# Performance work log

Hardware: AMD Instinct MI355X
Metric: run time of the kernel (lower is better)

Reference implementation:

```python
import jax, jax.numpy as jnp
import numpy as np

B, S, D_MODEL, D_K, D_V = 4, 2048, 1024, 1024, 1024


def setup_inputs() -> dict:
    key = jax.random.key(0)
    k1, k2, k3, k4 = jax.random.split(key, 4)
    scale = 1.0 / np.sqrt(D_MODEL)
    x = jax.random.normal(k1, (B, S, D_MODEL), dtype=jnp.float32)
    Wq = jax.random.normal(k2, (D_K, D_MODEL), dtype=jnp.float32) * scale
    Wk = jax.random.normal(k3, (D_K, D_MODEL), dtype=jnp.float32) * scale
    Wv = jax.random.normal(k4, (D_V, D_MODEL), dtype=jnp.float32) * scale
    # causal mask: position i may attend to j <= i (True = keep)
    mask = jnp.broadcast_to(jnp.tril(jnp.ones((S, S), dtype=bool)), (B, S, S))
    return {"x": x, "mask": mask, "Wq": Wq, "Wk": Wk, "Wv": Wv}


def reference(x, mask, Wq, Wk, Wv):
    # nn.Linear(d, k, bias=False): y = x @ W.T with W of shape [k, d]
    q = jnp.einsum('bsd,kd->bsk', x, Wq)
    k = jnp.einsum('bsd,kd->bsk', x, Wk)
    v = jnp.einsum('bsd,vd->bsv', x, Wv)
    scores = jnp.einsum('bik,bjk->bij', q, k) / jnp.sqrt(jnp.float32(D_K))
    s = jnp.where(mask, scores, -jnp.inf)
    # masked, fully-masked-row-safe softmax (fully masked rows -> all zeros,
    # matching softmax[all-masked rows] = 0 in the original)
    m = jnp.max(s, axis=-1, keepdims=True)
    m_safe = jnp.where(jnp.isfinite(m), m, 0.0)
    e = jnp.exp(s - m_safe)          # exp(-inf) = 0 for masked entries
    denom = jnp.sum(e, axis=-1, keepdims=True)
    p = e / jnp.where(denom == 0.0, 1.0, denom)
    return jnp.einsum('bij,bjv->biv', p, v)
```

## Files before the change

### kernel.cpp

```cpp
#include <hip/hip_runtime.h>
#include <hip/hip_bf16.h>
#include <stdint.h>

#define SEQ   2048
#define DM    1024
#define NBAT  4

typedef __attribute__((ext_vector_type(8))) short  short8;
typedef __attribute__((ext_vector_type(4))) float  floatx4;

__device__ __forceinline__ unsigned short f2b(float f) {
    __hip_bfloat16 h = __float2bfloat16(f);
    unsigned short r;
    __builtin_memcpy(&r, &h, 2);
    return r;
}

__device__ __forceinline__ ushort4 pack4(float a, float b, float c, float d) {
    ushort4 u; u.x = f2b(a); u.y = f2b(b); u.z = f2b(c); u.w = f2b(d); return u;
}

__device__ __forceinline__ void gload16(const void* g, void* s) {
    __builtin_amdgcn_global_load_lds(
        (const __attribute__((address_space(1))) unsigned int*)(uintptr_t)g,
        (__attribute__((address_space(3))) unsigned int*)(uintptr_t)s,
        16, 0, 0);
}

__global__ void prep(const float4* __restrict__ x,
                     const float4* __restrict__ w0, const float4* __restrict__ w1,
                     const float4* __restrict__ w2,
                     ushort4* __restrict__ xb, ushort4* __restrict__ wall,
                     float* __restrict__ rsum)
{
    const int b = blockIdx.x;
    const int t = threadIdx.x;
    if (b < 8192) {
        const int i = b * 256 + t;
        float4 f = x[i];
        xb[i] = pack4(f.x, f.y, f.z, f.w);
    } else if (b < 11264) {
        const int idx  = b - 8192;
        const int wsel = idx >> 10;
        const int i    = (idx & 1023) * 256 + t;
        const float4* src = (wsel == 0) ? w0 : (wsel == 1) ? w1 : w2;
        float4 f = src[i];
        wall[(size_t)wsel * 262144 + i] = pack4(f.x, f.y, f.z, f.w);
    } else {
        rsum[(b - 11264) * 256 + t] = 0.f;
    }
}

__global__ __launch_bounds__(256) void qkv_gemm(
    const unsigned short* __restrict__ A, const unsigned short* __restrict__ Bm,
    unsigned short* __restrict__ Qo, unsigned short* __restrict__ Ko,
    unsigned short* __restrict__ Vto, float qscale)
{
    const int m0 = blockIdx.y * 128;
    const int n0 = blockIdx.x * 128;
    const int K  = DM;

    __shared__ __align__(16) unsigned short As[128 * 64];
    __shared__ __align__(16) unsigned short Bs[128 * 64];

    const int t    = threadIdx.x;
    const int w    = t >> 6;
    const int lane = t & 63;
    const int wr   = w >> 1, wc = w & 1;
    const int r    = lane & 15, q = lane >> 4;

    floatx4 acc[4][4];
#pragma unroll
    for (int i = 0; i < 4; i++)
#pragma unroll
        for (int j = 0; j < 4; j++)
            acc[i][j] = (floatx4){0.f, 0.f, 0.f, 0.f};

    const int rr0 = t >> 3;
    const int pg  = (t & 7) ^ ((t >> 3) & 7);
    const int swz = r & 7;

    for (int k0 = 0; k0 < K; k0 += 64) {
        const size_t ka = (size_t)k0 + pg * 8;
#pragma unroll
        for (int g = 0; g < 4; g++) {
            gload16(A  + (size_t)(m0 + g * 32 + rr0) * K + ka, As + g * 2048 + (size_t)w * 512);
            gload16(Bm + (size_t)(n0 + g * 32 + rr0) * K + ka, Bs + g * 2048 + (size_t)w * 512);
        }
        __builtin_amdgcn_s_waitcnt(0);
        __syncthreads();

#pragma unroll
        for (int kk = 0; kk < 2; kk++) {
            short8 af[4], bf[4];
            const int slot = ((kk * 4 + q) ^ swz) * 8;
#pragma unroll
            for (int i = 0; i < 4; i++) {
                af[i] = *(const short8*)&As[(wr * 64 + i * 16 + r) * 64 + slot];
                bf[i] = *(const short8*)&Bs[(wc * 64 + i * 16 + r) * 64 + slot];
            }
#pragma unroll
            for (int i = 0; i < 4; i++)
#pragma unroll
                for (int j = 0; j < 4; j++)
                    acc[i][j] = __builtin_amdgcn_mfma_f32_16x16x32_bf16(af[i], bf[j], acc[i][j], 0, 0, 0);
        }
        __syncthreads();
    }

    const int gmb = m0 + wr * 64 + q * 4;
    const int gnb = n0 + wc * 64 + r;
#pragma unroll
    for (int i = 0; i < 4; i++) {
        const int gm = gmb + i * 16;
#pragma unroll
        for (int j = 0; j < 4; j++) {
            const int gn = gnb + j * 16;
            if (n0 < 1024) {
#pragma unroll
                for (int rr = 0; rr < 4; rr++)
                    Qo[(size_t)(gm + rr) * 1024 + gn] = f2b(acc[i][j][rr] * qscale);
            } else if (n0 < 2048) {
#pragma unroll
                for (int rr = 0; rr < 4; rr++)
                    Ko[(size_t)(gm + rr) * 1024 + (gn - 1024)] = f2b(acc[i][j][rr]);
            } else {
                const int b = gm >> 11;
                const int s = gm & 2047;
                const int v = gn - 2048;
                *(ushort4*)&Vto[((size_t)(b * 1024 + v)) * 2048 + s] =
                    pack4(acc[i][j][0], acc[i][j][1], acc[i][j][2], acc[i][j][3]);
            }
        }
    }
}

template<int MODE>
__global__ __launch_bounds__(256) void attn64(
    const unsigned short* __restrict__ Ag, const unsigned short* __restrict__ Bg,
    void* __restrict__ Cv, float* __restrict__ rowsum)
{
    const int z = blockIdx.z;
    int m0, n0;
    if (MODE == 0) {
        const int f = blockIdx.x;
        int ti = (int)((sqrtf(4.f * f + 1.f) - 1.f) * 0.5f);
        while ((ti + 1) * (ti + 2) <= f) ti++;
        while (ti * (ti + 1) > f) ti--;
        const int tj = f - ti * (ti + 1);
        m0 = ti * 128;
        n0 = tj * 64;
    } else {
        m0 = (int)(gridDim.y - 1 - blockIdx.y) * 128;
        n0 = blockIdx.x * 64;
    }

    const int lda = (MODE == 0) ? DM : SEQ;
    const int ldb = (MODE == 0) ? DM : SEQ;
    const unsigned short* A  = Ag + (size_t)z * ((MODE == 0) ? SEQ * DM : SEQ * SEQ);
    const unsigned short* Bm = Bg + (size_t)z * ((MODE == 0) ? SEQ * DM : DM * SEQ);
    const int kEnd = (MODE == 0) ? DM : (m0 + 128);

    __shared__ __align__(16) unsigned short As[128 * 64];
    __shared__ __align__(16) unsigned short Bs[64 * 64];

    const int t    = threadIdx.x;
    const int w    = t >> 6;
    const int lane = t & 63;
    const int r    = lane & 15, q = lane >> 4;

    floatx4 acc[2][4];
#pragma unroll
    for (int i = 0; i < 2; i++)
#pragma unroll
        for (int j = 0; j < 4; j++)
            acc[i][j] = (floatx4){0.f, 0.f, 0.f, 0.f};

    const int rr0 = t >> 3;
    const int pg  = (t & 7) ^ ((t >> 3) & 7);
    const int swz = r & 7;

    for (int k0 = 0; k0 < kEnd; k0 += 64) {
        const size_t ka = (size_t)k0 + pg * 8;
#pragma unroll
        for (int g = 0; g < 4; g++)
            gload16(A + (size_t)(m0 + g * 32 + rr0) * lda + ka,
                    As + g * 2048 + (size_t)w * 512);
#pragma unroll
        for (int g = 0; g < 2; g++)
            gload16(Bm + (size_t)(n0 + g * 32 + rr0) * ldb + ka,
                    Bs + g * 2048 + (size_t)w * 512);
        __builtin_amdgcn_s_waitcnt(0);
        __syncthreads();

#pragma unroll
        for (int kk = 0; kk < 2; kk++) {
            short8 af[2], bf[4];
            const int slot = ((kk * 4 + q) ^ swz) * 8;
#pragma unroll
            for (int i = 0; i < 2; i++)
                af[i] = *(const short8*)&As[(w * 32 + i * 16 + r) * 64 + slot];
#pragma unroll
            for (int j = 0; j < 4; j++)
                bf[j] = *(const short8*)&Bs[(j * 16 + r) * 64 + slot];
#pragma unroll
            for (int i = 0; i < 2; i++)
#pragma unroll
                for (int j = 0; j < 4; j++)
                    acc[i][j] = __builtin_amdgcn_mfma_f32_16x16x32_bf16(bf[j], af[i], acc[i][j], 0, 0, 0);
        }
        __syncthreads();
    }

    const int gmb = m0 + w * 32 + r;
    const int gnb = n0 + q * 4;
    if (MODE == 0) {
        unsigned short* E = (unsigned short*)Cv + (size_t)z * SEQ * SEQ;
        float* rs = rowsum + (size_t)z * SEQ;
#pragma unroll
        for (int i = 0; i < 2; i++) {
            const int gm = gmb + i * 16;
            float part = 0.f;
#pragma unroll
            for (int j = 0; j < 4; j++) {
                const int gn = gnb + j * 16;
                float e0 = (gn + 0 <= gm) ? __expf(acc[i][j][0]) : 0.f;
                float e1 = (gn + 1 <= gm) ? __expf(acc[i][j][1]) : 0.f;
                float e2 = (gn + 2 <= gm) ? __expf(acc[i][j][2]) : 0.f;
                float e3 = (gn + 3 <= gm) ? __expf(acc[i][j][3]) : 0.f;
                part += (e0 + e1) + (e2 + e3);
                *(ushort4*)&E[(size_t)gm * SEQ + gn] = pack4(e0, e1, e2, e3);
            }
            part += __shfl_xor(part, 16, 64);
            part += __shfl_xor(part, 32, 64);
            if (q == 0) atomicAdd(&rs[gm], part);
        }
    } else {
        float* C = (float*)Cv + (size_t)z * SEQ * DM;
        const float* rs = rowsum + (size_t)z * SEQ;
#pragma unroll
        for (int i = 0; i < 2; i++) {
            const int gm = gmb + i * 16;
            const float inv = 1.0f / rs[gm];
#pragma unroll
            for (int j = 0; j < 4; j++) {
                const int gn = gnb + j * 16;
                float4 o;
                o.x = acc[i][j][0] * inv;
                o.y = acc[i][j][1] * inv;
                o.z = acc[i][j][2] * inv;
                o.w = acc[i][j][3] * inv;
                *(float4*)&C[(size_t)gm * DM + gn] = o;
            }
        }
    }
}

extern "C" void kernel_launch(void* const* d_in, const int* in_sizes, int n_in,
                              void* d_out, int out_size, void* d_ws, size_t ws_size,
                              hipStream_t stream) {
    (void)in_sizes; (void)n_in; (void)out_size; (void)ws_size;
    const float* x  = (const float*)d_in[0];
    const float* Wq = (const float*)d_in[2];
    const float* Wk = (const float*)d_in[3];
    const float* Wv = (const float*)d_in[4];

    char* base = (char*)d_ws;
    size_t off = 0;
    auto alloc = [&](size_t n) { char* p = base + off; off += (n + 255) & ~(size_t)255; return p; };

    unsigned short* xb   = (unsigned short*)alloc((size_t)NBAT * SEQ * DM * 2);
    unsigned short* wall = (unsigned short*)alloc((size_t)3 * DM * DM * 2);
    unsigned short* Qb   = (unsigned short*)alloc((size_t)NBAT * SEQ * DM * 2);
    unsigned short* Kb   = (unsigned short*)alloc((size_t)NBAT * SEQ * DM * 2);
    unsigned short* Vtb  = (unsigned short*)alloc((size_t)NBAT * DM * SEQ * 2);
    unsigned short* E    = (unsigned short*)alloc((size_t)NBAT * SEQ * SEQ * 2);
    float*          rsum = (float*)alloc((size_t)NBAT * SEQ * 4);

    const dim3 blk(256);

    prep<<<dim3(11296), blk, 0, stream>>>(
        (const float4*)x, (const float4*)Wq, (const float4*)Wk, (const float4*)Wv,
        (ushort4*)xb, (ushort4*)wall, rsum);

    const int Mtot = NBAT * SEQ;

    qkv_gemm<<<dim3(3 * DM / 128, Mtot / 128, 1), blk, 0, stream>>>(
        xb, wall, Qb, Kb, Vtb, 0.03125f);

    attn64<0><<<dim3(272, 1, NBAT), blk, 0, stream>>>(Qb, Kb, E, rsum);

    attn64<1><<<dim3(DM / 64, SEQ / 128, NBAT), blk, 0, stream>>>(E, Vtb, d_out, rsum);
}
```

Before: 284.3 us.

## Rewrite QKV GEMM as 256x256 tile, 8-wave, double-buffered pipelined kernel

Replaces the 128x128 single-buffered QKV projection GEMM with a 256x256 tile run by 512 threads. The kernel double-buffers its LDS stages, interleaves async global->LDS loads with the MFMA phases, and uses s_setprio with split barriers. It also adds an XCD-aware block remapping and a new swizzle. The goal is to hide global load latency, raise reuse per loaded byte, and stop stalling on waitcnt(0) every k step. In exchange it uses 128KB of LDS and more registers per thread, and depends on the hand-tuned vmcnt counts being correct.

```diff
diff --git a/kernel.cpp b/kernel.cpp
--- a/kernel.cpp
+++ b/kernel.cpp
@@ -51,83 +51,150 @@
     }
 }
 
-__global__ __launch_bounds__(256) void qkv_gemm(
+__global__ __launch_bounds__(512, 2) void qkv_gemm(
     const unsigned short* __restrict__ A, const unsigned short* __restrict__ Bm,
     unsigned short* __restrict__ Qo, unsigned short* __restrict__ Ko,
     unsigned short* __restrict__ Vto, float qscale)
 {
-    const int m0 = blockIdx.y * 128;
-    const int n0 = blockIdx.x * 128;
-    const int K  = DM;
-
-    __shared__ __align__(16) unsigned short As[128 * 64];
-    __shared__ __align__(16) unsigned short Bs[128 * 64];
+    __shared__ __align__(16) unsigned short lds[65536];
+
+    const int bid = blockIdx.x;
+    const int wg  = (bid & 7) * 48 + (bid >> 3);
+    const int mt  = wg / 12, nt = wg - mt * 12;
+    const int m0  = mt * 256, n0 = nt * 256;
 
     const int t    = threadIdx.x;
     const int w    = t >> 6;
     const int lane = t & 63;
-    const int wr   = w >> 1, wc = w & 1;
+    const int wr   = w >> 2, wc = w & 3;
     const int r    = lane & 15, q = lane >> 4;
 
-    floatx4 acc[4][4];
-#pragma unroll
-    for (int i = 0; i < 4; i++)
+    const int frA = r * 32 + ((q ^ (r & 3) ^ ((r >> 2) & 3)) << 3);
+
+    const int srow = w * 32 + (lane >> 2);
+    const int spc  = ((lane & 3) ^ ((lane >> 2) & 3) ^ (lane >> 4)) << 3;
+
+    floatx4 acc[8][4];
+#pragma unroll
+    for (int i = 0; i < 8; i++)
 #pragma unroll
         for (int j = 0; j < 4; j++)
             acc[i][j] = (floatx4){0.f, 0.f, 0.f, 0.f};
 
-    const int rr0 = t >> 3;
-    const int pg  = (t & 7) ^ ((t >> 3) & 7);
-    const int swz = r & 7;
-
-    for (int k0 = 0; k0 < K; k0 += 64) {
-        const size_t ka = (size_t)k0 + pg * 8;
-#pragma unroll
-        for (int g = 0; g < 4; g++) {
-            gload16(A  + (size_t)(m0 + g * 32 + rr0) * K + ka, As + g * 2048 + (size_t)w * 512);
-            gload16(Bm + (size_t)(n0 + g * 32 + rr0) * K + ka, Bs + g * 2048 + (size_t)w * 512);
-        }
-        __builtin_amdgcn_s_waitcnt(0);
-        __syncthreads();
-
-#pragma unroll
-        for (int kk = 0; kk < 2; kk++) {
-            short8 af[4], bf[4];
-            const int slot = ((kk * 4 + q) ^ swz) * 8;
-#pragma unroll
-            for (int i = 0; i < 4; i++) {
-                af[i] = *(const short8*)&As[(wr * 64 + i * 16 + r) * 64 + slot];
-                bf[i] = *(const short8*)&Bs[(wc * 64 + i * 16 + r) * 64 + slot];
-            }
-#pragma unroll
-            for (int i = 0; i < 4; i++)
-#pragma unroll
-                for (int j = 0; j < 4; j++)
-                    acc[i][j] = __builtin_amdgcn_mfma_f32_16x16x32_bf16(af[i], bf[j], acc[i][j], 0, 0, 0);
-        }
-        __syncthreads();
-    }
-
-    const int gmb = m0 + wr * 64 + q * 4;
+    short8 bf0, bf1, bf2, bf3;
+
+#define APL(P,KH) (((P)*2+(KH)) * 8192)
+#define BPL(P,KH) (32768 + ((P)*2+(KH)) * 8192)
+
+#define STG(G, R0, KB, PL) do { \
+    gload16((G) + (((size_t)((R0) + srow))      << 10) + (KB) + spc, &lds[(PL) + (w*2+0)*512]); \
+    gload16((G) + (((size_t)((R0) + srow + 16)) << 10) + (KB) + spc, &lds[(PL) + (w*2+1)*512]); \
+  } while (0)
+
+#define PHASE(P, KH, MS, SG, SR0, SKB, SPL, DO_VM) do { \
+    const unsigned short* Ap = &lds[APL(P,KH)]; \
+    short8 af0 = *(const short8*)&Ap[((wr)*128 + (MS)*64 +  0)*32 + frA]; \
+    short8 af1 = *(const short8*)&Ap[((wr)*128 + (MS)*64 + 16)*32 + frA]; \
+    short8 af2 = *(const short8*)&Ap[((wr)*128 + (MS)*64 + 32)*32 + frA]; \
+    short8 af3 = *(const short8*)&Ap[((wr)*128 + (MS)*64 + 48)*32 + frA]; \
+    if ((MS) == 0) { \
+        const unsigned short* Bp = &lds[BPL(P,KH)]; \
+        bf0 = *(const short8*)&Bp[((wc)*64 +  0)*32 + frA]; \
+        bf1 = *(const short8*)&Bp[((wc)*64 + 16)*32 + frA]; \
+        bf2 = *(const short8*)&Bp[((wc)*64 + 32)*32 + frA]; \
+        bf3 = *(const short8*)&Bp[((wc)*64 + 48)*32 + frA]; \
+    } \
+    STG(SG, SR0, SKB, SPL); \
+    __builtin_amdgcn_s_barrier(); \
+    asm volatile("s_waitcnt lgkmcnt(0)" ::: "memory"); \
+    __builtin_amdgcn_s_setprio(1); \
+    acc[(MS)*4+0][0] = __builtin_amdgcn_mfma_f32_16x16x32_bf16(af0, bf0, acc[(MS)*4+0][0], 0, 0, 0); \
+    acc[(MS)*4+0][1] = __builtin_amdgcn_mfma_f32_16x16x32_bf16(af0, bf1, acc[(MS)*4+0][1], 0, 0, 0); \
+    acc[(MS)*4+0][2] = __builtin_amdgcn_mfma_f32_16x16x32_bf16(af0, bf2, acc[(MS)*4+0][2], 0, 0, 0); \
+    acc[(MS)*4+0][3] = __builtin_amdgcn_mfma_f32_16x16x32_bf16(af0, bf3, acc[(MS)*4+0][3], 0, 0, 0); \
+    acc[(MS)*4+1][0] = __builtin_amdgcn_mfma_f32_16x16x32_bf16(af1, bf0, acc[(MS)*4+1][0], 0, 0, 0); \
+    acc[(MS)*4+1][1] = __builtin_amdgcn_mfma_f32_16x16x32_bf16(af1, bf1, acc[(MS)*4+1][1], 0, 0, 0); \
+    acc[(MS)*4+1][2] = __builtin_amdgcn_mfma_f32_16x16x32_bf16(af1, bf2, acc[(MS)*4+1][2], 0, 0, 0); \
+    acc[(MS)*4+1][3] = __builtin_amdgcn_mfma_f32_16x16x32_bf16(af1, bf3, acc[(MS)*4+1][3], 0, 0, 0); \
+    acc[(MS)*4+2][0] = __builtin_amdgcn_mfma_f32_16x16x32_bf16(af2, bf0, acc[(MS)*4+2][0], 0, 0, 0); \
+    acc[(MS)*4+2][1] = __builtin_amdgcn_mfma_f32_16x16x32_bf16(af2, bf1, acc[(MS)*4+2][1], 0, 0, 0); \
+    acc[(MS)*4+2][2] = __builtin_amdgcn_mfma_f32_16x16x32_bf16(af2, bf2, acc[(MS)*4+2][2], 0, 0, 0); \
+    acc[(MS)*4+2][3] = __builtin_amdgcn_mfma_f32_16x16x32_bf16(af2, bf3, acc[(MS)*4+2][3], 0, 0, 0); \
+    acc[(MS)*4+3][0] = __builtin_amdgcn_mfma_f32_16x16x32_bf16(af3, bf0, acc[(MS)*4+3][0], 0, 0, 0); \
+    acc[(MS)*4+3][1] = __builtin_amdgcn_mfma_f32_16x16x32_bf16(af3, bf1, acc[(MS)*4+3][1], 0, 0, 0); \
+    acc[(MS)*4+3][2] = __builtin_amdgcn_mfma_f32_16x16x32_bf16(af3, bf2, acc[(MS)*4+3][2], 0, 0, 0); \
+    acc[(MS)*4+3][3] = __builtin_amdgcn_mfma_f32_16x16x32_bf16(af3, bf3, acc[(MS)*4+3][3], 0, 0, 0); \
+    __builtin_amdgcn_s_setprio(0); \
+    if (DO_VM) asm volatile("s_waitcnt vmcnt(8)" ::: "memory"); \
+    __builtin_amdgcn_s_barrier(); \
+  } while (0)
+
+#define TILE(P, KB1, KB2) do { \
+    PHASE(P, 0, 0, A,  m0, (KB1) + 32, APL(1-(P),1), 0); \
+    PHASE(P, 0, 1, Bm, n0, (KB1) + 32, BPL(1-(P),1), 1); \
+    PHASE(P, 1, 0, A,  m0, (KB2),      APL(P,0),     0); \
+    PHASE(P, 1, 1, Bm, n0, (KB2),      BPL(P,0),     1); \
+  } while (0)
+
+    STG(A,  m0, 0,  APL(0,0));
+    STG(Bm, n0, 0,  BPL(0,0));
+    STG(A,  m0, 32, APL(0,1));
+    STG(Bm, n0, 32, BPL(0,1));
+    STG(A,  m0, 64, APL(1,0));
+    STG(Bm, n0, 64, BPL(1,0));
+    asm volatile("s_waitcnt vmcnt(8)" ::: "memory");
+    __builtin_amdgcn_s_barrier();
+
+    for (int tt = 0; tt < 16; tt += 2) {
+        const int kb1a = (tt + 1) * 64;
+        const int kb2a = (tt + 2 < 16 ? tt + 2 : 0) * 64;
+        TILE(0, kb1a, kb2a);
+        const int kb1b = kb2a;
+        const int kb2b = (tt + 3 < 16 ? tt + 3 : tt - 13) * 64;
+        TILE(1, kb1b, kb2b);
+    }
+
+#undef TILE
+#undef PHASE
+#undef STG
+#undef APL
+#undef BPL
+
+    const int gmb = m0 + wr * 128 + q * 4;
     const int gnb = n0 + wc * 64 + r;
-#pragma unroll
-    for (int i = 0; i < 4; i++) {
-        const int gm = gmb + i * 16;
-#pragma unroll
-        for (int j = 0; j < 4; j++) {
-            const int gn = gnb + j * 16;
-            if (n0 < 1024) {
+    if (nt < 4) {
+#pragma unroll
+        for (int i = 0; i < 8; i++) {
+            const int gm = gmb + i * 16;
+#pragma unroll
+            for (int j = 0; j < 4; j++) {
+                const int gn = gnb + j * 16;
 #pragma unroll
                 for (int rr = 0; rr < 4; rr++)
                     Qo[(size_t)(gm + rr) * 1024 + gn] = f2b(acc[i][j][rr] * qscale);
-            } else if (n0 < 2048) {
+            }
+        }
+    } else if (nt < 8) {
+#pragma unroll
+        for (int i = 0; i < 8; i++) {
+            const int gm = gmb + i * 16;
+#pragma unroll
+            for (int j = 0; j < 4; j++) {
+                const int gn = gnb + j * 16;
 #pragma unroll
                 for (int rr = 0; rr < 4; rr++)
                     Ko[(size_t)(gm + rr) * 1024 + (gn - 1024)] = f2b(acc[i][j][rr]);
-            } else {
-                const int b = gm >> 11;
-                const int s = gm & 2047;
-                const int v = gn - 2048;
+            }
+        }
+    } else {
+#pragma unroll
+        for (int i = 0; i < 8; i++) {
+            const int gm = gmb + i * 16;
+            const int b  = gm >> 11;
+            const int s  = gm & 2047;
+#pragma unroll
+            for (int j = 0; j < 4; j++) {
+                const int v = gnb + j * 16 - 2048;
                 *(ushort4*)&Vto[((size_t)(b * 1024 + v)) * 2048 + s] =
                     pack4(acc[i][j][0], acc[i][j][1], acc[i][j][2], acc[i][j][3]);
             }
@@ -283,9 +350,7 @@
         (const float4*)x, (const float4*)Wq, (const float4*)Wk, (const float4*)Wv,
         (ushort4*)xb, (ushort4*)wall, rsum);
 
-    const int Mtot = NBAT * SEQ;
-
-    qkv_gemm<<<dim3(3 * DM / 128, Mtot / 128, 1), blk, 0, stream>>>(
+    qkv_gemm<<<dim3(384), dim3(512), 0, stream>>>(
         xb, wall, Qb, Kb, Vtb, 0.03125f);
 
     attn64<0><<<dim3(272, 1, NBAT), blk, 0, stream>>>(Qb, Kb, E, rsum);
```

After: 283.7 us. About the same (-0.2%).

## Restructure QKV GEMM with 256x128 tiles, 512 threads and 5-stage LDS pipeline

Applied to the files above, without the earlier changes.

The QKV projection GEMM now uses 512-thread blocks computing 256x128 output tiles. A 5-slot LDS ring buffer prefetches four K-steps of 32 ahead with global_load_lds, and waits use explicit vmcnt counts instead of a full drain. Blocks are remapped with an XCD-aware swizzle over a 1D grid, the LDS layout uses a new XOR swizzle, and s_setprio is raised around the MFMA burst. The aim is to hide global-load latency and improve L2 reuse, at the cost of much more LDS per block (about 120KB) and possibly lower occupancy.

```diff
diff --git a/kernel.cpp b/kernel.cpp
--- a/kernel.cpp
+++ b/kernel.cpp
@@ -51,17 +51,19 @@
     }
 }
 
-__global__ __launch_bounds__(256) void qkv_gemm(
+#define SLOT 12288
+
+__global__ __launch_bounds__(512, 2) void qkv_gemm(
     const unsigned short* __restrict__ A, const unsigned short* __restrict__ Bm,
     unsigned short* __restrict__ Qo, unsigned short* __restrict__ Ko,
     unsigned short* __restrict__ Vto, float qscale)
 {
-    const int m0 = blockIdx.y * 128;
-    const int n0 = blockIdx.x * 128;
-    const int K  = DM;
-
-    __shared__ __align__(16) unsigned short As[128 * 64];
-    __shared__ __align__(16) unsigned short Bs[128 * 64];
+    __shared__ __align__(16) unsigned short lds[5 * SLOT];
+
+    const int bid = blockIdx.x;
+    const int wg  = (bid & 7) * 96 + (bid >> 3);
+    const int mt  = wg / 24, nt = wg - mt * 24;
+    const int m0  = mt * 256, n0 = nt * 128;
 
     const int t    = threadIdx.x;
     const int w    = t >> 6;
@@ -69,6 +71,16 @@
     const int wr   = w >> 1, wc = w & 1;
     const int r    = lane & 15, q = lane >> 4;
 
+    const int rp      = (r & ~1) | ((r ^ (r >> 1)) & 1);
+    const int fr      = (r & 3) ^ ((r >> 2) & 3);
+    const int laneOff = rp * 32 + ((q ^ fr) << 3);
+
+    const int R   = t >> 2;
+    const int sR  = (R & ~1) | ((R ^ (R >> 1)) & 1);
+    const int fS  = (sR & 3) ^ ((sR >> 2) & 3);
+    const int jS  = ((t & 3) ^ fS) << 3;
+    const int wS  = w * 512;
+
     floatx4 acc[4][4];
 #pragma unroll
     for (int i = 0; i < 4; i++)
@@ -76,58 +88,102 @@
         for (int j = 0; j < 4; j++)
             acc[i][j] = (floatx4){0.f, 0.f, 0.f, 0.f};
 
-    const int rr0 = t >> 3;
-    const int pg  = (t & 7) ^ ((t >> 3) & 7);
-    const int swz = r & 7;
-
-    for (int k0 = 0; k0 < K; k0 += 64) {
-        const size_t ka = (size_t)k0 + pg * 8;
-#pragma unroll
-        for (int g = 0; g < 4; g++) {
-            gload16(A  + (size_t)(m0 + g * 32 + rr0) * K + ka, As + g * 2048 + (size_t)w * 512);
-            gload16(Bm + (size_t)(n0 + g * 32 + rr0) * K + ka, Bs + g * 2048 + (size_t)w * 512);
-        }
-        __builtin_amdgcn_s_waitcnt(0);
-        __syncthreads();
-
-#pragma unroll
-        for (int kk = 0; kk < 2; kk++) {
-            short8 af[4], bf[4];
-            const int slot = ((kk * 4 + q) ^ swz) * 8;
-#pragma unroll
-            for (int i = 0; i < 4; i++) {
-                af[i] = *(const short8*)&As[(wr * 64 + i * 16 + r) * 64 + slot];
-                bf[i] = *(const short8*)&Bs[(wc * 64 + i * 16 + r) * 64 + slot];
-            }
-#pragma unroll
-            for (int i = 0; i < 4; i++)
-#pragma unroll
-                for (int j = 0; j < 4; j++)
-                    acc[i][j] = __builtin_amdgcn_mfma_f32_16x16x32_bf16(af[i], bf[j], acc[i][j], 0, 0, 0);
-        }
-        __syncthreads();
-    }
+#define STG3(T4, DSTS) do { \
+    const int kb_ = ((T4) < 32) ? (T4) * 32 : 0; \
+    gload16(A  + (((size_t)(m0 +       sR)) << 10) + kb_ + jS, &lds[(DSTS) +        wS]); \
+    gload16(A  + (((size_t)(m0 + 128 + sR)) << 10) + kb_ + jS, &lds[(DSTS) + 4096 + wS]); \
+    gload16(Bm + (((size_t)(n0 +       sR)) << 10) + kb_ + jS, &lds[(DSTS) + 8192 + wS]); \
+  } while (0)
+
+    STG3(0, 0 * SLOT);
+    STG3(1, 1 * SLOT);
+    STG3(2, 2 * SLOT);
+    STG3(3, 3 * SLOT);
+    asm volatile("s_waitcnt vmcnt(9)" ::: "memory");
+    __builtin_amdgcn_s_barrier();
+
+    int p = 0, q4 = 4;
+    for (int tt = 0; tt < 32; ++tt) {
+        const int slotS = p * SLOT;
+        const int aBase = slotS + wr * 4096 + laneOff;
+        const int aB = slotS + (wr >> 1) * 4096 + (wr & 1) * 2048 + laneOff;
+        const int bB = slotS + 8192 + wc * 2048 + laneOff;
+        (void)aBase;
+
+        short8 af0 = *(const short8*)&lds[aB +    0];
+        short8 af1 = *(const short8*)&lds[aB +  512];
+        short8 af2 = *(const short8*)&lds[aB + 1024];
+        short8 af3 = *(const short8*)&lds[aB + 1536];
+        short8 bf0 = *(const short8*)&lds[bB +    0];
+        short8 bf1 = *(const short8*)&lds[bB +  512];
+        short8 bf2 = *(const short8*)&lds[bB + 1024];
+        short8 bf3 = *(const short8*)&lds[bB + 1536];
+
+        STG3(tt + 4, q4 * SLOT);
+
+        asm volatile("s_waitcnt vmcnt(9)" ::: "memory");
+        __builtin_amdgcn_s_barrier();
+        asm volatile("s_waitcnt lgkmcnt(0)" ::: "memory");
+        __builtin_amdgcn_s_setprio(1);
+        acc[0][0] = __builtin_amdgcn_mfma_f32_16x16x32_bf16(af0, bf0, acc[0][0], 0, 0, 0);
+        acc[0][1] = __builtin_amdgcn_mfma_f32_16x16x32_bf16(af0, bf1, acc[0][1], 0, 0, 0);
+        acc[0][2] = __builtin_amdgcn_mfma_f32_16x16x32_bf16(af0, bf2, acc[0][2], 0, 0, 0);
+        acc[0][3] = __builtin_amdgcn_mfma_f32_16x16x32_bf16(af0, bf3, acc[0][3], 0, 0, 0);
+        acc[1][0] = __builtin_amdgcn_mfma_f32_16x16x32_bf16(af1, bf0, acc[1][0], 0, 0, 0);
+        acc[1][1] = __builtin_amdgcn_mfma_f32_16x16x32_bf16(af1, bf1, acc[1][1], 0, 0, 0);
+        acc[1][2] = __builtin_amdgcn_mfma_f32_16x16x32_bf16(af1, bf2, acc[1][2], 0, 0, 0);
+        acc[1][3] = __builtin_amdgcn_mfma_f32_16x16x32_bf16(af1, bf3, acc[1][3], 0, 0, 0);
+        acc[2][0] = __builtin_amdgcn_mfma_f32_16x16x32_bf16(af2, bf0, acc[2][0], 0, 0, 0);
+        acc[2][1] = __builtin_amdgcn_mfma_f32_16x16x32_bf16(af2, bf1, acc[2][1], 0, 0, 0);
+        acc[2][2] = __builtin_amdgcn_mfma_f32_16x16x32_bf16(af2, bf2, acc[2][2], 0, 0, 0);
+        acc[2][3] = __builtin_amdgcn_mfma_f32_16x16x32_bf16(af2, bf3, acc[2][3], 0, 0, 0);
+        acc[3][0] = __builtin_amdgcn_mfma_f32_16x16x32_bf16(af3, bf0, acc[3][0], 0, 0, 0);
+        acc[3][1] = __builtin_amdgcn_mfma_f32_16x16x32_bf16(af3, bf1, acc[3][1], 0, 0, 0);
+        acc[3][2] = __builtin_amdgcn_mfma_f32_16x16x32_bf16(af3, bf2, acc[3][2], 0, 0, 0);
+        acc[3][3] = __builtin_amdgcn_mfma_f32_16x16x32_bf16(af3, bf3, acc[3][3], 0, 0, 0);
+        __builtin_amdgcn_s_setprio(0);
+        __builtin_amdgcn_s_barrier();
+
+        p  = (p  == 4) ? 0 : p  + 1;
+        q4 = (q4 == 4) ? 0 : q4 + 1;
+    }
+#undef STG3
 
     const int gmb = m0 + wr * 64 + q * 4;
     const int gnb = n0 + wc * 64 + r;
-#pragma unroll
-    for (int i = 0; i < 4; i++) {
-        const int gm = gmb + i * 16;
-#pragma unroll
-        for (int j = 0; j < 4; j++) {
-            const int gn = gnb + j * 16;
-            if (n0 < 1024) {
+    if (nt < 8) {
+#pragma unroll
+        for (int i = 0; i < 4; i++) {
+            const int gm = gmb + i * 16;
+#pragma unroll
+            for (int j = 0; j < 4; j++) {
+                const int gn = gnb + j * 16;
 #pragma unroll
                 for (int rr = 0; rr < 4; rr++)
                     Qo[(size_t)(gm + rr) * 1024 + gn] = f2b(acc[i][j][rr] * qscale);
-            } else if (n0 < 2048) {
+            }
+        }
+    } else if (nt < 16) {
+#pragma unroll
+        for (int i = 0; i < 4; i++) {
+            const int gm = gmb + i * 16;
+#pragma unroll
+            for (int j = 0; j < 4; j++) {
+                const int gn = gnb + j * 16;
 #pragma unroll
                 for (int rr = 0; rr < 4; rr++)
                     Ko[(size_t)(gm + rr) * 1024 + (gn - 1024)] = f2b(acc[i][j][rr]);
-            } else {
-                const int b = gm >> 11;
-                const int s = gm & 2047;
-                const int v = gn - 2048;
+            }
+        }
+    } else {
+#pragma unroll
+        for (int i = 0; i < 4; i++) {
+            const int gm = gmb + i * 16;
+            const int b  = gm >> 11;
+            const int s  = gm & 2047;
+#pragma unroll
+            for (int j = 0; j < 4; j++) {
+                const int v = gnb + j * 16 - 2048;
                 *(ushort4*)&Vto[((size_t)(b * 1024 + v)) * 2048 + s] =
                     pack4(acc[i][j][0], acc[i][j][1], acc[i][j][2], acc[i][j][3]);
             }
@@ -283,9 +339,7 @@
         (const float4*)x, (const float4*)Wq, (const float4*)Wk, (const float4*)Wv,
         (ushort4*)xb, (ushort4*)wall, rsum);
 
-    const int Mtot = NBAT * SEQ;
-
-    qkv_gemm<<<dim3(3 * DM / 128, Mtot / 128, 1), blk, 0, stream>>>(
+    qkv_gemm<<<dim3(768), dim3(512), 0, stream>>>(
         xb, wall, Qb, Kb, Vtb, 0.03125f);
 
     attn64<0><<<dim3(272, 1, NBAT), blk, 0, stream>>>(Qb, Kb, E, rsum);
```

New measurement: 280.8 us. About the same (-1.2%).

## Replace GEMMs with 256x256 double-buffered 8-wave kernel and split-K PV

Applied to the files above, without the earlier changes.

All three GEMM stages now share one templated kernel that uses 256x256 output tiles, 512 threads and double-buffered LDS (128 KB). Global-to-LDS loads for the next k-step are interleaved with MFMA phases under setprio and barriers. The QKV GEMM uses an XCD-aware block remap. The PV stage splits long causal rows into two K-halves that accumulate with float atomics into an output pre-zeroed by the prep kernel. The aim is higher MFMA utilisation and more data reuse per tile, at the cost of one block per CU, coarser causal tiling that computes more masked work, and atomic traffic.

```diff
diff --git a/kernel.cpp b/kernel.cpp
--- a/kernel.cpp
+++ b/kernel.cpp
@@ -31,7 +31,7 @@
                      const float4* __restrict__ w0, const float4* __restrict__ w1,
                      const float4* __restrict__ w2,
                      ushort4* __restrict__ xb, ushort4* __restrict__ wall,
-                     float* __restrict__ rsum)
+                     float* __restrict__ rsum, float4* __restrict__ outz)
 {
     const int b = blockIdx.x;
     const int t = threadIdx.x;
@@ -46,179 +46,210 @@
         const float4* src = (wsel == 0) ? w0 : (wsel == 1) ? w1 : w2;
         float4 f = src[i];
         wall[(size_t)wsel * 262144 + i] = pack4(f.x, f.y, f.z, f.w);
+    } else if (b < 11296) {
+        rsum[(b - 11264) * 256 + t] = 0.f;
     } else {
-        rsum[(b - 11264) * 256 + t] = 0.f;
-    }
-}
-
-__global__ __launch_bounds__(256) void qkv_gemm(
-    const unsigned short* __restrict__ A, const unsigned short* __restrict__ Bm,
-    unsigned short* __restrict__ Qo, unsigned short* __restrict__ Ko,
-    unsigned short* __restrict__ Vto, float qscale)
+        const int u = b - 11296;
+        const int z = u >> 10, idx = u & 1023;
+        outz[(size_t)z * 524288 + 262144 + idx * 256 + t] = (float4){0.f, 0.f, 0.f, 0.f};
+    }
+}
+
+template<int EPI>
+__global__ __launch_bounds__(512, 2) void gemm8p(
+    const unsigned short* __restrict__ Ag, const unsigned short* __restrict__ Bg,
+    void* __restrict__ P0, void* __restrict__ P1, void* __restrict__ P2,
+    float* __restrict__ rowsum, float qscale)
 {
-    const int m0 = blockIdx.y * 128;
-    const int n0 = blockIdx.x * 128;
-    const int K  = DM;
-
-    __shared__ __align__(16) unsigned short As[128 * 64];
-    __shared__ __align__(16) unsigned short Bs[128 * 64];
+    __shared__ __align__(16) unsigned short lds[65536];
+
+    int m0, n0, start, cnt, ntl = 0, z = 0, atom = 0;
+    const unsigned short* A;
+    const unsigned short* Bm;
+    size_t LDA, LDB;
+
+    if (EPI == 0) {
+        const int bid = blockIdx.x;
+        const int wg  = (bid & 7) * 48 + (bid >> 3);
+        const int mt  = wg / 12; ntl = wg - mt * 12;
+        m0 = mt * 256; n0 = ntl * 256;
+        A = Ag; Bm = Bg; LDA = DM; LDB = DM; start = 0; cnt = 16;
+    } else if (EPI == 1) {
+        z = blockIdx.z;
+        const int f = blockIdx.x;
+        int ti = (int)((sqrtf(8.f * f + 1.f) - 1.f) * 0.5f);
+        while ((ti + 1) * (ti + 2) / 2 <= f) ti++;
+        while (ti * (ti + 1) / 2 > f) ti--;
+        const int tj = f - ti * (ti + 1) / 2;
+        m0 = ti * 256; n0 = tj * 256;
+        A = Ag + (size_t)z * SEQ * DM; Bm = Bg + (size_t)z * SEQ * DM;
+        LDA = DM; LDB = DM; start = 0; cnt = 16;
+    } else {
+        z = blockIdx.z;
+        const int wrk = blockIdx.x;
+        int ti, seg;
+        if (wrk < 4) { ti = wrk; seg = -1; start = 0; cnt = 4 * (ti + 1); atom = 0; }
+        else { const int e = wrk - 4; ti = 4 + (e >> 1); seg = e & 1;
+               const int NT = 4 * (ti + 1); cnt = NT >> 1; start = seg * cnt; atom = 1; }
+        m0 = ti * 256; n0 = blockIdx.y * 256;
+        A = Ag + (size_t)z * SEQ * SEQ; Bm = Bg + (size_t)z * DM * SEQ;
+        LDA = SEQ; LDB = SEQ;
+    }
 
     const int t    = threadIdx.x;
     const int w    = t >> 6;
     const int lane = t & 63;
-    const int wr   = w >> 1, wc = w & 1;
+    const int wr   = w >> 2, wc = w & 3;
     const int r    = lane & 15, q = lane >> 4;
 
-    floatx4 acc[4][4];
-#pragma unroll
-    for (int i = 0; i < 4; i++)
+    const int srow = lane >> 3;
+    const int scol = ((lane & 7) ^ srow) << 3;
+
+    const int sk0 = ((0 + q) ^ (r & 7)) * 8;
+    const int sk1 = ((4 + q) ^ (r & 7)) * 8;
+    const int aRd = wr * 8192 + r * 64;
+    const int bRd = 16384 + (wc >> 1) * 8192 + ((wc & 1) * 64 + r) * 64;
+
+    floatx4 acc[8][4];
+#pragma unroll
+    for (int i = 0; i < 8; i++)
 #pragma unroll
         for (int j = 0; j < 4; j++)
             acc[i][j] = (floatx4){0.f, 0.f, 0.f, 0.f};
 
-    const int rr0 = t >> 3;
-    const int pg  = (t & 7) ^ ((t >> 3) & 7);
-    const int swz = r & 7;
-
-    for (int k0 = 0; k0 < K; k0 += 64) {
-        const size_t ka = (size_t)k0 + pg * 8;
-#pragma unroll
-        for (int g = 0; g < 4; g++) {
-            gload16(A  + (size_t)(m0 + g * 32 + rr0) * K + ka, As + g * 2048 + (size_t)w * 512);
-            gload16(Bm + (size_t)(n0 + g * 32 + rr0) * K + ka, Bs + g * 2048 + (size_t)w * 512);
+#define STGC(G, R0, LD, KB, CB) do { \
+    gload16((G) + (size_t)((R0) + w * 16 + srow)     * (LD) + (KB) + scol, &lds[(CB) + w * 1024]); \
+    gload16((G) + (size_t)((R0) + w * 16 + srow + 8) * (LD) + (KB) + scol, &lds[(CB) + w * 1024 + 512]); \
+  } while (0)
+
+#define RD_A(IB, SK) do { \
+    af0 = *(const short8*)&lds[cb + aRd + ((IB) + 0) * 1024 + (SK)]; \
+    af1 = *(const short8*)&lds[cb + aRd + ((IB) + 1) * 1024 + (SK)]; \
+    af2 = *(const short8*)&lds[cb + aRd + ((IB) + 2) * 1024 + (SK)]; \
+    af3 = *(const short8*)&lds[cb + aRd + ((IB) + 3) * 1024 + (SK)]; \
+  } while (0)
+#define RD_B(SK) do { \
+    bf0 = *(const short8*)&lds[cb + bRd + 0 * 1024 + (SK)]; \
+    bf1 = *(const short8*)&lds[cb + bRd + 1 * 1024 + (SK)]; \
+    bf2 = *(const short8*)&lds[cb + bRd + 2 * 1024 + (SK)]; \
+    bf3 = *(const short8*)&lds[cb + bRd + 3 * 1024 + (SK)]; \
+  } while (0)
+
+#define ONE_MFMA(AC, AF, BF) do { \
+    if (EPI == 0) (AC) = __builtin_amdgcn_mfma_f32_16x16x32_bf16((AF), (BF), (AC), 0, 0, 0); \
+    else          (AC) = __builtin_amdgcn_mfma_f32_16x16x32_bf16((BF), (AF), (AC), 0, 0, 0); \
+  } while (0)
+#define MFMA16(IB) do { \
+    ONE_MFMA(acc[(IB)+0][0], af0, bf0); ONE_MFMA(acc[(IB)+0][1], af0, bf1); \
+    ONE_MFMA(acc[(IB)+0][2], af0, bf2); ONE_MFMA(acc[(IB)+0][3], af0, bf3); \
+    ONE_MFMA(acc[(IB)+1][0], af1, bf0); ONE_MFMA(acc[(IB)+1][1], af1, bf1); \
+    ONE_MFMA(acc[(IB)+1][2], af1, bf2); ONE_MFMA(acc[(IB)+1][3], af1, bf3); \
+    ONE_MFMA(acc[(IB)+2][0], af2, bf0); ONE_MFMA(acc[(IB)+2][1], af2, bf1); \
+    ONE_MFMA(acc[(IB)+2][2], af2, bf2); ONE_MFMA(acc[(IB)+2][3], af2, bf3); \
+    ONE_MFMA(acc[(IB)+3][0], af3, bf0); ONE_MFMA(acc[(IB)+3][1], af3, bf1); \
+    ONE_MFMA(acc[(IB)+3][2], af3, bf2); ONE_MFMA(acc[(IB)+3][3], af3, bf3); \
+  } while (0)
+
+#define PH_SYNC() do { \
+    __builtin_amdgcn_s_barrier(); \
+    asm volatile("s_waitcnt lgkmcnt(0)" ::: "memory"); \
+    __builtin_amdgcn_sched_barrier(0); \
+    __builtin_amdgcn_s_setprio(1); \
+  } while (0)
+#define PH_END() do { \
+    __builtin_amdgcn_s_setprio(0); \
+    __builtin_amdgcn_s_barrier(); \
+  } while (0)
+
+    {
+        const int kb = start * 64;
+        STGC(A,  m0,       LDA, kb, 0);
+        STGC(A,  m0 + 128, LDA, kb, 8192);
+        STGC(Bm, n0,       LDB, kb, 16384);
+        STGC(Bm, n0 + 128, LDB, kb, 24576);
+        asm volatile("s_waitcnt vmcnt(0)" ::: "memory");
+        __builtin_amdgcn_s_barrier();
+    }
+
+    short8 af0, af1, af2, af3, bf0, bf1, bf2, bf3;
+
+    for (int tt = 0; tt < cnt; ++tt) {
+        const int cb  = (tt & 1) * 32768;
+        const int ob  = 32768 - cb;
+        const int nkb = (tt + 1 < cnt ? start + tt + 1 : start) * 64;
+
+        RD_A(0, sk0); RD_B(sk0);
+        STGC(A, m0,       LDA, nkb, ob);
+        STGC(A, m0 + 128, LDA, nkb, ob + 8192);
+        PH_SYNC(); MFMA16(0); PH_END();
+
+        RD_A(4, sk0);
+        STGC(Bm, n0,       LDB, nkb, ob + 16384);
+        STGC(Bm, n0 + 128, LDB, nkb, ob + 24576);
+        PH_SYNC(); MFMA16(4); PH_END();
+
+        RD_A(0, sk1); RD_B(sk1);
+        PH_SYNC(); MFMA16(0); PH_END();
+
+        RD_A(4, sk1);
+        asm volatile("s_waitcnt vmcnt(0)" ::: "memory");
+        PH_SYNC(); MFMA16(4); PH_END();
+    }
+#undef STGC
+#undef RD_A
+#undef RD_B
+
+    if (EPI == 0) {
+        const int gmb = m0 + wr * 128 + q * 4;
+        const int gnb = n0 + wc * 64 + r;
+        unsigned short* Qo  = (unsigned short*)P0;
+        unsigned short* Ko  = (unsigned short*)P1;
+        unsigned short* Vto = (unsigned short*)P2;
+        if (ntl < 4) {
+#pragma unroll
+            for (int i = 0; i < 8; i++) {
+                const int gm = gmb + i * 16;
+#pragma unroll
+                for (int j = 0; j < 4; j++) {
+                    const int gn = gnb + j * 16;
+#pragma unroll
+                    for (int rr = 0; rr < 4; rr++)
+                        Qo[(size_t)(gm + rr) * 1024 + gn] = f2b(acc[i][j][rr] * qscale);
+                }
+            }
+        } else if (ntl < 8) {
+#pragma unroll
+            for (int i = 0; i < 8; i++) {
+                const int gm = gmb + i * 16;
+#pragma unroll
+                for (int j = 0; j < 4; j++) {
+                    const int gn = gnb + j * 16;
+#pragma unroll
+                    for (int rr = 0; rr < 4; rr++)
+                        Ko[(size_t)(gm + rr) * 1024 + (gn - 1024)] = f2b(acc[i][j][rr]);
+                }
+            }
+        } else {
+#pragma unroll
+            for (int i = 0; i < 8; i++) {
+                const int gm = gmb + i * 16;
+                const int b  = gm >> 11;
+                const int s  = gm & 2047;
+#pragma unroll
+                for (int j = 0; j < 4; j++) {
+                    const int v = gnb + j * 16 - 2048;
+                    *(ushort4*)&Vto[((size_t)(b * 1024 + v)) * 2048 + s] =
+                        pack4(acc[i][j][0], acc[i][j][1], acc[i][j][2], acc[i][j][3]);
+                }
+            }
         }
-        __builtin_amdgcn_s_waitcnt(0);
-        __syncthreads();
-
-#pragma unroll
-        for (int kk = 0; kk < 2; kk++) {
-            short8 af[4], bf[4];
-            const int slot = ((kk * 4 + q) ^ swz) * 8;
-#pragma unroll
-            for (int i = 0; i < 4; i++) {
-                af[i] = *(const short8*)&As[(wr * 64 + i * 16 + r) * 64 + slot];
-                bf[i] = *(const short8*)&Bs[(wc * 64 + i * 16 + r) * 64 + slot];
-            }
-#pragma unroll
-            for (int i = 0; i < 4; i++)
-#pragma unroll
-                for (int j = 0; j < 4; j++)
-                    acc[i][j] = __builtin_amdgcn_mfma_f32_16x16x32_bf16(af[i], bf[j], acc[i][j], 0, 0, 0);
-        }
-        __syncthreads();
-    }
-
-    const int gmb = m0 + wr * 64 + q * 4;
-    const int gnb = n0 + wc * 64 + r;
-#pragma unroll
-    for (int i = 0; i < 4; i++) {
-        const int gm = gmb + i * 16;
-#pragma unroll
-        for (int j = 0; j < 4; j++) {
-            const int gn = gnb + j * 16;
-            if (n0 < 1024) {
-#pragma unroll
-                for (int rr = 0; rr < 4; rr++)
-                    Qo[(size_t)(gm + rr) * 1024 + gn] = f2b(acc[i][j][rr] * qscale);
-            } else if (n0 < 2048) {
-#pragma unroll
-                for (int rr = 0; rr < 4; rr++)
-                    Ko[(size_t)(gm + rr) * 1024 + (gn - 1024)] = f2b(acc[i][j][rr]);
-            } else {
-                const int b = gm >> 11;
-                const int s = gm & 2047;
-                const int v = gn - 2048;
-                *(ushort4*)&Vto[((size_t)(b * 1024 + v)) * 2048 + s] =
-                    pack4(acc[i][j][0], acc[i][j][1], acc[i][j][2], acc[i][j][3]);
-            }
-        }
-    }
-}
-
-template<int MODE>
-__global__ __launch_bounds__(256) void attn64(
-    const unsigned short* __restrict__ Ag, const unsigned short* __restrict__ Bg,
-    void* __restrict__ Cv, float* __restrict__ rowsum)
-{
-    const int z = blockIdx.z;
-    int m0, n0;
-    if (MODE == 0) {
-        const int f = blockIdx.x;
-        int ti = (int)((sqrtf(4.f * f + 1.f) - 1.f) * 0.5f);
-        while ((ti + 1) * (ti + 2) <= f) ti++;
-        while (ti * (ti + 1) > f) ti--;
-        const int tj = f - ti * (ti + 1);
-        m0 = ti * 128;
-        n0 = tj * 64;
-    } else {
-        m0 = (int)(gridDim.y - 1 - blockIdx.y) * 128;
-        n0 = blockIdx.x * 64;
-    }
-
-    const int lda = (MODE == 0) ? DM : SEQ;
-    const int ldb = (MODE == 0) ? DM : SEQ;
-    const unsigned short* A  = Ag + (size_t)z * ((MODE == 0) ? SEQ * DM : SEQ * SEQ);
-    const unsigned short* Bm = Bg + (size_t)z * ((MODE == 0) ? SEQ * DM : DM * SEQ);
-    const int kEnd = (MODE == 0) ? DM : (m0 + 128);
-
-    __shared__ __align__(16) unsigned short As[128 * 64];
-    __shared__ __align__(16) unsigned short Bs[64 * 64];
-
-    const int t    = threadIdx.x;
-    const int w    = t >> 6;
-    const int lane = t & 63;
-    const int r    = lane & 15, q = lane >> 4;
-
-    floatx4 acc[2][4];
-#pragma unroll
-    for (int i = 0; i < 2; i++)
-#pragma unroll
-        for (int j = 0; j < 4; j++)
-            acc[i][j] = (floatx4){0.f, 0.f, 0.f, 0.f};
-
-    const int rr0 = t >> 3;
-    const int pg  = (t & 7) ^ ((t >> 3) & 7);
-    const int swz = r & 7;
-
-    for (int k0 = 0; k0 < kEnd; k0 += 64) {
-        const size_t ka = (size_t)k0 + pg * 8;
-#pragma unroll
-        for (int g = 0; g < 4; g++)
-            gload16(A + (size_t)(m0 + g * 32 + rr0) * lda + ka,
-                    As + g * 2048 + (size_t)w * 512);
-#pragma unroll
-        for (int g = 0; g < 2; g++)
-            gload16(Bm + (size_t)(n0 + g * 32 + rr0) * ldb + ka,
-                    Bs + g * 2048 + (size_t)w * 512);
-        __builtin_amdgcn_s_waitcnt(0);
-        __syncthreads();
-
-#pragma unroll
-        for (int kk = 0; kk < 2; kk++) {
-            short8 af[2], bf[4];
-            const int slot = ((kk * 4 + q) ^ swz) * 8;
-#pragma unroll
-            for (int i = 0; i < 2; i++)
-                af[i] = *(const short8*)&As[(w * 32 + i * 16 + r) * 64 + slot];
-#pragma unroll
-            for (int j = 0; j < 4; j++)
-                bf[j] = *(const short8*)&Bs[(j * 16 + r) * 64 + slot];
-#pragma unroll
-            for (int i = 0; i < 2; i++)
-#pragma unroll
-                for (int j = 0; j < 4; j++)
-                    acc[i][j] = __builtin_amdgcn_mfma_f32_16x16x32_bf16(bf[j], af[i], acc[i][j], 0, 0, 0);
-        }
-        __syncthreads();
-    }
-
-    const int gmb = m0 + w * 32 + r;
-    const int gnb = n0 + q * 4;
-    if (MODE == 0) {
-        unsigned short* E = (unsigned short*)Cv + (size_t)z * SEQ * SEQ;
+    } else if (EPI == 1) {
+        const int gmb = m0 + wr * 128 + r;
+        const int gnb = n0 + wc * 64 + q * 4;
+        unsigned short* E = (unsigned short*)P0 + (size_t)z * SEQ * SEQ;
         float* rs = rowsum + (size_t)z * SEQ;
 #pragma unroll
-        for (int i = 0; i < 2; i++) {
+        for (int i = 0; i < 8; i++) {
             const int gm = gmb + i * 16;
             float part = 0.f;
 #pragma unroll
@@ -236,21 +267,33 @@
             if (q == 0) atomicAdd(&rs[gm], part);
         }
     } else {
-        float* C = (float*)Cv + (size_t)z * SEQ * DM;
+        const int gmb = m0 + wr * 128 + r;
+        const int gnb = n0 + wc * 64 + q * 4;
+        float* C = (float*)P0 + (size_t)z * SEQ * DM;
         const float* rs = rowsum + (size_t)z * SEQ;
 #pragma unroll
-        for (int i = 0; i < 2; i++) {
+        for (int i = 0; i < 8; i++) {
             const int gm = gmb + i * 16;
             const float inv = 1.0f / rs[gm];
-#pragma unroll
-            for (int j = 0; j < 4; j++) {
-                const int gn = gnb + j * 16;
-                float4 o;
-                o.x = acc[i][j][0] * inv;
-                o.y = acc[i][j][1] * inv;
-                o.z = acc[i][j][2] * inv;
-                o.w = acc[i][j][3] * inv;
-                *(float4*)&C[(size_t)gm * DM + gn] = o;
+            if (atom) {
+#pragma unroll
+                for (int j = 0; j < 4; j++) {
+                    const int gn = gnb + j * 16;
+#pragma unroll
+                    for (int rr = 0; rr < 4; rr++)
+                        atomicAdd(&C[(size_t)gm * DM + gn + rr], acc[i][j][rr] * inv);
+                }
+            } else {
+#pragma unroll
+                for (int j = 0; j < 4; j++) {
+                    const int gn = gnb + j * 16;
+                    float4 o;
+                    o.x = acc[i][j][0] * inv;
+                    o.y = acc[i][j][1] * inv;
+                    o.z = acc[i][j][2] * inv;
+                    o.w = acc[i][j][3] * inv;
+                    *(float4*)&C[(size_t)gm * DM + gn] = o;
+                }
             }
         }
     }
@@ -277,18 +320,16 @@
     unsigned short* E    = (unsigned short*)alloc((size_t)NBAT * SEQ * SEQ * 2);
     float*          rsum = (float*)alloc((size_t)NBAT * SEQ * 4);
 
-    const dim3 blk(256);
-
-    prep<<<dim3(11296), blk, 0, stream>>>(
+    prep<<<dim3(15392), dim3(256), 0, stream>>>(
         (const float4*)x, (const float4*)Wq, (const float4*)Wk, (const float4*)Wv,
-        (ushort4*)xb, (ushort4*)wall, rsum);
-
-    const int Mtot = NBAT * SEQ;
-
-    qkv_gemm<<<dim3(3 * DM / 128, Mtot / 128, 1), blk, 0, stream>>>(
-        xb, wall, Qb, Kb, Vtb, 0.03125f);
-
-    attn64<0><<<dim3(272, 1, NBAT), blk, 0, stream>>>(Qb, Kb, E, rsum);
-
-    attn64<1><<<dim3(DM / 64, SEQ / 128, NBAT), blk, 0, stream>>>(E, Vtb, d_out, rsum);
-}
+        (ushort4*)xb, (ushort4*)wall, rsum, (float4*)d_out);
+
+    gemm8p<0><<<dim3(384), dim3(512), 0, stream>>>(
+        xb, wall, Qb, Kb, Vtb, nullptr, 0.03125f);
+
+    gemm8p<1><<<dim3(36, 1, NBAT), dim3(512), 0, stream>>>(
+        Qb, Kb, E, nullptr, nullptr, rsum, 0.f);
+
+    gemm8p<2><<<dim3(12, 4, NBAT), dim3(512), 0, stream>>>(
+        E, Vtb, d_out, nullptr, nullptr, rsum, 0.f);
+}
```

Result: slower. 356.1 us (+25.3%).
